# Optimization experiments

Measured on AMD Instinct MI355X. Metric: run time of the kernel, lower is better.

## Reference

```python
import jax, jax.numpy as jnp
import numpy as np

T, D, H, KEXP = 91, 256, 4, 4
DH = D // H
NA, NRG = 128, 1024
NEG = -1e10
SCALE = 2.0  # sqrt(head_num=4), faithful to the original (NOT sqrt(dh))


def _ln(x, g, b, eps=1e-5):
    m = jnp.mean(x, axis=-1, keepdims=True)
    v = jnp.mean((x - m) ** 2, axis=-1, keepdims=True)
    return (x - m) * jax.lax.rsqrt(v + eps) * g + b


def setup_inputs() -> dict:
    key = jax.random.key(0)
    ks = jax.random.split(key, 16)
    s = lambda fan_in: 1.0 / np.sqrt(fan_in)
    inp = {
        "agent": jax.random.normal(ks[0], (NA, T, D), jnp.float32),
        "rg": jax.random.normal(ks[1], (NRG, T, D), jnp.float32),
        "ln_x_g": jnp.ones((D,), jnp.float32),
        "ln_x_b": jnp.zeros((D,), jnp.float32),
        "wk": jax.random.uniform(ks[2], (D, D), jnp.float32, -s(D), s(D)),
        "bk": jnp.zeros((D,), jnp.float32),
        "wv": jax.random.uniform(ks[3], (D, D), jnp.float32, -s(D), s(D)),
        "bv": jnp.zeros((D,), jnp.float32),
        "wq": jax.random.uniform(ks[4], (D, D), jnp.float32, -s(D), s(D)),
        "bq": jnp.zeros((D,), jnp.float32),
        "q_scale": jnp.full((DH,), 0.001, jnp.float32),
        "wy": jax.random.uniform(ks[5], (D, D), jnp.float32, -s(D), s(D)),
        "by": jnp.zeros((D,), jnp.float32),
        "wf1": jax.random.uniform(ks[6], (D, KEXP * D), jnp.float32, -s(D), s(D)),
        "bf1": jnp.zeros((KEXP * D,), jnp.float32),
        "wf2": jax.random.uniform(ks[7], (KEXP * D, D), jnp.float32, -s(KEXP * D), s(KEXP * D)),
        "bf2": jnp.zeros((D,), jnp.float32),
        "ln_z_g": jnp.ones((D,), jnp.float32),
        "ln_z_b": jnp.zeros((D,), jnp.float32),
        "agent_rg_mask": jax.random.randint(ks[8], (T, NA, NRG), 0, 2).astype(bool),
        "padding_mask": jax.random.randint(ks[9], (T, NRG), 0, 2).astype(bool),
        "rg_valid_mask": jax.random.randint(ks[10], (T, NA), 0, 2).astype(bool),
    }
    return inp


def reference(agent, rg, ln_x_g, ln_x_b, wk, bk, wv, bv, wq, bq, q_scale,
              wy, by, wf1, bf1, wf2, bf2, ln_z_g, ln_z_b,
              agent_rg_mask, padding_mask, rg_valid_mask):
    agent_n = _ln(agent, ln_x_g, ln_x_b)   # (Na, T, D)
    rg_n = _ln(rg, ln_x_g, ln_x_b)         # (Nrg, T, D)

    K = jax.nn.relu(rg_n @ wk + bk).reshape(NRG, T, H, DH)
    V = jax.nn.relu(rg_n @ wv + bv).reshape(NRG, T, H, DH)
    Q = jax.nn.relu(agent_n @ wq + bq).reshape(NA, T, H, DH) * q_scale

    # energy: (T, H, Na, Nrg)
    energy = jnp.einsum("athd,rthd->thar", Q, K) / SCALE
    energy = jnp.where(agent_rg_mask[:, None, :, :], energy, NEG)
    energy = jnp.where(padding_mask[:, None, None, :], energy, NEG)
    energy = jnp.where(rg_valid_mask[:, None, :, None], energy, NEG)
    attn = jax.nn.softmax(energy, axis=-1)

    Y1 = jnp.einsum("thar,rthd->athd", attn, V).reshape(NA, T, D)
    Y2 = jax.nn.relu(Y1 @ wy + by)
    S = Y2 + agent_n
    F1 = jax.nn.relu(S @ wf1 + bf1)
    F2 = jax.nn.relu(F1 @ wf2 + bf2)
    Z = _ln(F2, ln_z_g, ln_z_b)

    Qp = jnp.transpose(Q, (1, 2, 0, 3))  # (T,H,Na,dh)
    Kp = jnp.transpose(K, (1, 2, 0, 3))
    Vp = jnp.transpose(V, (1, 2, 0, 3))
    return (Z, Qp, Kp, Vp)
```

## Files before the change

kernel.cpp:

```cpp
#include <hip/hip_runtime.h>

#define T_   91
#define D_   256
#define H_   4
#define DH_  64
#define NA_  128
#define NRG_ 1024
#define KEXP_ 4

typedef float f32x4 __attribute__((ext_vector_type(4)));
typedef short bf16x8 __attribute__((ext_vector_type(8)));

static constexpr float P_EPS = 1.3877787807814457e-17f;

__device__ inline ushort f2bf(float f) {
    union { float f; unsigned u; } v; v.f = f;
    unsigned r = (v.u + 0x7fffu + ((v.u >> 16) & 1u)) >> 16;
    return (ushort)r;
}
__device__ inline unsigned pk2(float a, float b) {
    return (unsigned)f2bf(a) | ((unsigned)f2bf(b) << 16);
}
__device__ inline float bf2f(ushort b) {
    union { unsigned u; float f; } v; v.u = ((unsigned)b) << 16;
    return v.f;
}

#define LN_BLOCKS 2912
#define PM_BLOCKS 2912
#define PW_BLOCKS 3072
#define KV_BLOCKS 2912

__global__ __launch_bounds__(256) void prep_all(
    const float* __restrict__ agent,
    const float* __restrict__ g, const float* __restrict__ b,
    const int* __restrict__ am, const int* __restrict__ pm,
    const int* __restrict__ vmk,
    const float* __restrict__ wk, const float* __restrict__ wv,
    const float* __restrict__ wq, const float* __restrict__ wy,
    const float* __restrict__ wf1, const float* __restrict__ wf2,
    ushort* __restrict__ agn, unsigned* __restrict__ cm,
    ushort* __restrict__ wkvt, ushort* __restrict__ wqt,
    ushort* __restrict__ wyt, ushort* __restrict__ wf1t,
    ushort* __restrict__ wf2t) {
    __shared__ int pmS[NRG_];
    int bid = blockIdx.x;
    if (bid < LN_BLOCKS) {
        int row = bid * 4 + (threadIdx.x >> 6);
        int lane = threadIdx.x & 63;
        f32x4 x = *(const f32x4*)(agent + (size_t)row * D_ + lane * 4);
        float s1 = x[0] + x[1] + x[2] + x[3];
        float s2 = x[0] * x[0] + x[1] * x[1] + x[2] * x[2] + x[3] * x[3];
#pragma unroll
        for (int off = 1; off < 64; off <<= 1) {
            s1 += __shfl_xor(s1, off);
            s2 += __shfl_xor(s2, off);
        }
        float mean = s1 * (1.0f / 256.0f);
        float var = s2 * (1.0f / 256.0f) - mean * mean;
        float rstd = rsqrtf(var + 1e-5f);
        f32x4 gv = *(const f32x4*)(g + lane * 4);
        f32x4 bv = *(const f32x4*)(b + lane * 4);
        float y0 = (x[0] - mean) * rstd * gv[0] + bv[0];
        float y1 = (x[1] - mean) * rstd * gv[1] + bv[1];
        float y2 = (x[2] - mean) * rstd * gv[2] + bv[2];
        float y3 = (x[3] - mean) * rstd * gv[3] + bv[3];
        *(uint2*)(agn + (size_t)row * D_ + lane * 4) =
            make_uint2(pk2(y0, y1), pk2(y2, y3));
    } else if (bid < LN_BLOCKS + PM_BLOCKS) {
        int base = (bid - LN_BLOCKS) * 4;
        int t = base / NA_;
        int w = threadIdx.x >> 6, lane = threadIdx.x & 63;
#pragma unroll
        for (int i = 0; i < 4; ++i)
            pmS[threadIdx.x + i * 256] = pm[(size_t)t * NRG_ + threadIdx.x + i * 256];
        __syncthreads();
        int idx = base + w;
        int a = idx & (NA_ - 1);
        int valid = vmk[t * NA_ + a];
        const int* amrow = am + (size_t)idx * NRG_;
#pragma unroll
        for (int c = 0; c < 16; ++c) {
            int r = c * 64 + lane;
            bool bit = valid && amrow[r] && pmS[r];
            unsigned long long msk = __ballot(bit);
            if (lane == 0) {
                cm[(size_t)idx * 32 + c * 2]     = (unsigned)msk;
                cm[(size_t)idx * 32 + c * 2 + 1] = (unsigned)(msk >> 32);
            }
        }
    } else {
        int idx = (bid - LN_BLOCKS - PM_BLOCKS) * 256 + threadIdx.x;
        if (idx < 131072) {
            const float* W = (idx < 65536) ? wk : wv;
            int li = idx & 65535;
            int n = li >> 8, k = li & 255;
            wkvt[idx] = f2bf(W[(size_t)k * 256 + n]);
        } else if (idx < 196608) {
            int li = idx - 131072;
            int n = li >> 8, k = li & 255;
            wqt[li] = f2bf(wq[(size_t)k * 256 + n]);
        } else if (idx < 262144) {
            int li = idx - 196608;
            int n = li >> 8, k = li & 255;
            wyt[li] = f2bf(wy[(size_t)k * 256 + n]);
        } else if (idx < 524288) {
            int li = idx - 262144;
            int n = li >> 8, k = li & 255;
            wf1t[li] = f2bf(wf1[(size_t)k * 1024 + n]);
        } else {
            int li = idx - 524288;
            int n = li >> 10, k = li & 1023;
            wf2t[li] = f2bf(wf2[(size_t)k * 256 + n]);
        }
    }
}

__global__ __launch_bounds__(512) void gemm_kvq(
    const float* __restrict__ rgf, const ushort* __restrict__ agn,
    const float* __restrict__ lng, const float* __restrict__ lnb,
    const ushort* __restrict__ wkvt, const ushort* __restrict__ wqt,
    const float* __restrict__ bk, const float* __restrict__ bv,
    const float* __restrict__ bq, const float* __restrict__ qs,
    float* __restrict__ Kp, float* __restrict__ Vp, float* __restrict__ Qp,
    ushort* __restrict__ Kb, ushort* __restrict__ Vtb, ushort* __restrict__ Qb) {
    __shared__ ushort Asf[64][264];
    __shared__ ushort Bs[256][72];

    int bid = blockIdx.x;
    bool isQ = bid >= KV_BLOCKS;
    int bxi = 0, t, rb = 0, a0 = 0;
    if (!isQ) {
        int sub = bid & 15, pid = bid >> 4;
        bxi = sub >> 3;
        int by = pid * 8 + (sub & 7);
        t = by >> 4; rb = (by & 15) << 6;
    } else {
        int qid = bid - KV_BLOCKS;
        t = qid >> 1; a0 = (qid & 1) << 6;
    }
    const ushort* Bt = isQ ? wqt : (wkvt + (size_t)(bxi << 8) * 256);

    int tid = threadIdx.x;
    int w = tid >> 6, lane = tid & 63;
    int wm = w >> 2, wn = w & 3;
    int l15 = lane & 15, l4 = lane >> 4;

    if (!isQ) {
        int row = tid >> 3, l8 = tid & 7;
        const float* ap = rgf + ((size_t)(rb + row) * T_ + t) * 256;
        f32x4 xr[8];
#pragma unroll
        for (int c = 0; c < 8; ++c) xr[c] = *(const f32x4*)(ap + l8 * 4 + c * 32);
        float s1 = 0.0f, s2 = 0.0f;
#pragma unroll
        for (int c = 0; c < 8; ++c)
#pragma unroll
            for (int r = 0; r < 4; ++r) { s1 += xr[c][r]; s2 += xr[c][r] * xr[c][r]; }
#pragma unroll
        for (int off = 1; off < 8; off <<= 1) {
            s1 += __shfl_xor(s1, off);
            s2 += __shfl_xor(s2, off);
        }
        float mean = s1 * (1.0f / 256.0f);
        float var = s2 * (1.0f / 256.0f) - mean * mean;
        float rstd = rsqrtf(var + 1e-5f);
#pragma unroll
        for (int c = 0; c < 8; ++c) {
            int col = l8 * 4 + c * 32;
            f32x4 g4 = *(const f32x4*)(lng + col);
            f32x4 b4 = *(const f32x4*)(lnb + col);
            float y0 = (xr[c][0] - mean) * rstd * g4[0] + b4[0];
            float y1 = (xr[c][1] - mean) * rstd * g4[1] + b4[1];
            float y2 = (xr[c][2] - mean) * rstd * g4[2] + b4[2];
            float y3 = (xr[c][3] - mean) * rstd * g4[3] + b4[3];
            *(uint2*)&Asf[row][col] = make_uint2(pk2(y0, y1), pk2(y2, y3));
        }
    } else {
#pragma unroll
        for (int i2 = 0; i2 < 4; ++i2) {
            int chunk = tid + i2 * 512;
            int row = chunk >> 5, c8 = (chunk & 31) * 8;
            *(bf16x8*)&Asf[row][c8] =
                *(const bf16x8*)(agn + ((size_t)(a0 + row) * T_ + t) * 256 + c8);
        }
    }

    f32x4 acc[2][4];
#pragma unroll
    for (int i = 0; i < 2; ++i)
#pragma unroll
        for (int j = 0; j < 4; ++j)
#pragma unroll
            for (int r = 0; r < 4; ++r) acc[i][j][r] = 0.0f;

    for (int k0 = 0; k0 < 256; k0 += 64) {
#pragma unroll
        for (int it = 0; it < 4; ++it) {
            int li = tid + it * 512;
            int row = li >> 3, c8 = (li & 7) * 8;
            *(bf16x8*)&Bs[row][c8] =
                *(const bf16x8*)(Bt + (size_t)row * 256 + k0 + c8);
        }
        __syncthreads();
#pragma unroll
        for (int kk = 0; kk < 2; ++kk) {
            bf16x8 af[2], bfr[4];
#pragma unroll
            for (int i = 0; i < 2; ++i)
                af[i] = *(const bf16x8*)&Asf[wm * 32 + i * 16 + l15][k0 + kk * 32 + l4 * 8];
#pragma unroll
            for (int j = 0; j < 4; ++j)
                bfr[j] = *(const bf16x8*)&Bs[wn * 64 + j * 16 + l15][kk * 32 + l4 * 8];
#pragma unroll
            for (int i = 0; i < 2; ++i)
#pragma unroll
                for (int j = 0; j < 4; ++j)
                    acc[i][j] = __builtin_amdgcn_mfma_f32_16x16x32_bf16(
                        af[i], bfr[j], acc[i][j], 0, 0, 0);
        }
        __syncthreads();
    }

#pragma unroll
    for (int i = 0; i < 2; ++i)
#pragma unroll
        for (int j = 0; j < 4; ++j) {
            int n = wn * 64 + j * 16 + l15;
            int h = n >> 6, d = n & 63;
            int m0 = wm * 32 + i * 16 + l4 * 4;
            float vv[4];
#pragma unroll
            for (int reg = 0; reg < 4; ++reg) {
                float bs = isQ ? bq[n] : (bxi ? bv[n] : bk[n]);
                float x = fmaxf(acc[i][j][reg] + bs, 0.0f);
                if (isQ) x *= qs[d];
                vv[reg] = x;
            }
            if (isQ) {
                size_t base = (((size_t)t * H_ + h) * NA_ + a0) * DH_ + d;
#pragma unroll
                for (int reg = 0; reg < 4; ++reg) {
                    Qp[base + (size_t)(m0 + reg) * DH_] = vv[reg];
                    Qb[base + (size_t)(m0 + reg) * DH_] = f2bf(vv[reg] * 0.5f);
                }
            } else if (!bxi) {
                size_t base = (((size_t)t * H_ + h) * NRG_ + rb) * DH_ + d;
#pragma unroll
                for (int reg = 0; reg < 4; ++reg) {
                    Kp[base + (size_t)(m0 + reg) * DH_] = vv[reg];
                    Kb[base + (size_t)(m0 + reg) * DH_] = f2bf(vv[reg]);
                }
            } else {
                size_t base = (((size_t)t * H_ + h) * NRG_ + rb) * DH_ + d;
#pragma unroll
                for (int reg = 0; reg < 4; ++reg)
                    Vp[base + (size_t)(m0 + reg) * DH_] = vv[reg];
                size_t tb = ((size_t)t * H_ + h) * DH_ * NRG_;
                *(uint2*)(Vtb + tb + (size_t)d * NRG_ + rb + m0) =
                    make_uint2(pk2(vv[0], vv[1]), pk2(vv[2], vv[3]));
            }
        }
}

__global__ __launch_bounds__(512) void gemm_wide(
    const ushort* __restrict__ Ab, const ushort* __restrict__ Bt,
    const float* __restrict__ bias0, const float* __restrict__ bias1,
    const float* __restrict__ aux0, const ushort* __restrict__ residb,
    float* __restrict__ out0, ushort* __restrict__ out2,
    int N, int K, int mode) {
    __shared__ ushort smem[64 * 72 + 256 * 72];
    __shared__ float lnp[2][64][4];
    ushort (*As)[72] = (ushort(*)[72])smem;
    ushort (*Bs)[72] = (ushort(*)[72])(smem + 64 * 72);
    float (*Et)[68] = (float(*)[68])smem;

    int bxi = blockIdx.x, by = blockIdx.y;
    int bn = bxi * 256, bm = by * 64;

    int tid = threadIdx.x;
    int w = tid >> 6, lane = tid & 63;
    int wm = w >> 2, wn = w & 3;
    int l15 = lane & 15, l4 = lane >> 4;

    f32x4 acc[2][4];
#pragma unroll
    for (int i = 0; i < 2; ++i)
#pragma unroll
        for (int j = 0; j < 4; ++j)
#pragma unroll
            for (int r = 0; r < 4; ++r) acc[i][j][r] = 0.0f;

    for (int k0 = 0; k0 < K; k0 += 64) {
        {
            int row = tid >> 3, c8 = (tid & 7) * 8;
            *(bf16x8*)&As[row][c8] =
                *(const bf16x8*)(Ab + (size_t)(bm + row) * K + k0 + c8);
        }
#pragma unroll
        for (int it = 0; it < 4; ++it) {
            int li = tid + it * 512;
            int row = li >> 3, c8 = (li & 7) * 8;
            *(bf16x8*)&Bs[row][c8] =
                *(const bf16x8*)(Bt + (size_t)(bn + row) * K + k0 + c8);
        }
        __syncthreads();
#pragma unroll
        for (int kk = 0; kk < 2; ++kk) {
            bf16x8 af[2], bfr[4];
#pragma unroll
            for (int i = 0; i < 2; ++i)
                af[i] = *(const bf16x8*)&As[wm * 32 + i * 16 + l15][kk * 32 + l4 * 8];
#pragma unroll
            for (int j = 0; j < 4; ++j)
                bfr[j] = *(const bf16x8*)&Bs[wn * 64 + j * 16 + l15][kk * 32 + l4 * 8];
#pragma unroll
            for (int i = 0; i < 2; ++i)
#pragma unroll
                for (int j = 0; j < 4; ++j)
                    acc[i][j] = __builtin_amdgcn_mfma_f32_16x16x32_bf16(
                        af[i], bfr[j], acc[i][j], 0, 0, 0);
        }
        __syncthreads();
    }

    float v[2][4][4];
#pragma unroll
    for (int i = 0; i < 2; ++i)
#pragma unroll
        for (int j = 0; j < 4; ++j)
#pragma unroll
            for (int reg = 0; reg < 4; ++reg) {
                int nl = wn * 64 + j * 16 + l15;
                int rowl = wm * 32 + i * 16 + l4 * 4 + reg;
                float bs = (mode == 0) ? bias0[bn + nl] : bias0[nl];
                float x = fmaxf(acc[i][j][reg] + bs, 0.0f);
                if (mode == 3) x += bf2f(residb[(size_t)(bm + rowl) * 256 + nl]);
                v[i][j][reg] = x;
            }

    if (mode == 5) {
        float rs_[2][4], rq_[2][4];
#pragma unroll
        for (int i = 0; i < 2; ++i)
#pragma unroll
            for (int reg = 0; reg < 4; ++reg) {
                float s = 0.0f, q = 0.0f;
#pragma unroll
                for (int j = 0; j < 4; ++j) {
                    float x = v[i][j][reg];
                    s += x; q += x * x;
                }
#pragma unroll
                for (int off = 1; off < 16; off <<= 1) {
                    s += __shfl_xor(s, off);
                    q += __shfl_xor(q, off);
                }
                rs_[i][reg] = s; rq_[i][reg] = q;
            }
        if (l15 == 0) {
#pragma unroll
            for (int i = 0; i < 2; ++i)
#pragma unroll
                for (int reg = 0; reg < 4; ++reg) {
                    int row = wm * 32 + i * 16 + l4 * 4 + reg;
                    lnp[0][row][wn] = rs_[i][reg];
                    lnp[1][row][wn] = rq_[i][reg];
                }
        }
        __syncthreads();
#pragma unroll
        for (int i = 0; i < 2; ++i)
#pragma unroll
            for (int reg = 0; reg < 4; ++reg) {
                int row = wm * 32 + i * 16 + l4 * 4 + reg;
                float S1 = lnp[0][row][0] + lnp[0][row][1] + lnp[0][row][2] + lnp[0][row][3];
                float S2 = lnp[1][row][0] + lnp[1][row][1] + lnp[1][row][2] + lnp[1][row][3];
                float mean = S1 * (1.0f / 256.0f);
                float var = S2 * (1.0f / 256.0f) - mean * mean;
                float rstd = rsqrtf(var + 1e-5f);
#pragma unroll
                for (int j = 0; j < 4; ++j) {
                    int nl = wn * 64 + j * 16 + l15;
                    float z = (v[i][j][reg] - mean) * rstd * bias1[nl] + aux0[nl];
                    out0[(size_t)(bm + row) * 256 + nl] = z;
                }
            }
        return;
    }

#pragma unroll 1
    for (int jq = 0; jq < 4; ++jq) {
        __syncthreads();
        if (wn == jq) {
#pragma unroll
            for (int i = 0; i < 2; ++i)
#pragma unroll
                for (int j = 0; j < 4; ++j)
#pragma unroll
                    for (int reg = 0; reg < 4; ++reg)
                        Et[wm * 32 + i * 16 + l4 * 4 + reg][j * 16 + l15] = v[i][j][reg];
        }
        __syncthreads();
#pragma unroll
        for (int it = 0; it < 2; ++it) {
            int slot = it * 512 + tid;
            int row = slot >> 4, c4 = (slot & 15) * 4;
            uint2 u = make_uint2(pk2(Et[row][c4], Et[row][c4 + 1]),
                                 pk2(Et[row][c4 + 2], Et[row][c4 + 3]));
            *(uint2*)(out2 + (size_t)(bm + row) * N + bn + jq * 64 + c4) = u;
        }
    }
}

__global__ __launch_bounds__(512) void attn_flash(
    const ushort* __restrict__ Qb, const ushort* __restrict__ Kb,
    const ushort* __restrict__ Vtb, const unsigned* __restrict__ cm,
    ushort* __restrict__ Y1b) {
    int th = blockIdx.x;
    int t = th >> 2, h = th & 3;
    int tid = threadIdx.x;
    int w = tid >> 6, lane = tid & 63;
    int l15 = lane & 15, l4 = lane >> 4;

    __shared__ ushort Ks[2][64][72];
    __shared__ ushort Vts[2][64][72];
    __shared__ ushort Ps[128][72];
    __shared__ unsigned cmAll[128][33];

    bf16x8 qf[2];
#pragma unroll
    for (int kk = 0; kk < 2; ++kk)
        qf[kk] = *(const bf16x8*)(Qb + ((size_t)th * NA_ + w * 16 + l15) * DH_
                                  + kk * 32 + l4 * 8);

    {
        const uint4* src = (const uint4*)(cm + (size_t)t * NA_ * 32 + tid * 8);
        uint4 c0 = src[0], c1 = src[1];
        int a = tid >> 2, wd = (tid & 3) * 8;
        cmAll[a][wd + 0] = c0.x; cmAll[a][wd + 1] = c0.y;
        cmAll[a][wd + 2] = c0.z; cmAll[a][wd + 3] = c0.w;
        cmAll[a][wd + 4] = c1.x; cmAll[a][wd + 5] = c1.y;
        cmAll[a][wd + 6] = c1.z; cmAll[a][wd + 7] = c1.w;
    }

    int srow = tid >> 3, sc8 = (tid & 7) * 8;
    const ushort* Kbase = Kb + (size_t)th * NRG_ * DH_;
    const ushort* Vbase = Vtb + (size_t)th * DH_ * NRG_;
    bf16x8 kreg = *(const bf16x8*)(Kbase + (size_t)srow * DH_ + sc8);
    bf16x8 vreg = *(const bf16x8*)(Vbase + (size_t)srow * NRG_ + sc8);
    *(bf16x8*)&Ks[0][srow][sc8] = kreg;
    *(bf16x8*)&Vts[0][srow][sc8] = vreg;
    __syncthreads();

    f32x4 o[4];
    float rsum[4] = {0.0f, 0.0f, 0.0f, 0.0f};
#pragma unroll
    for (int ds = 0; ds < 4; ++ds)
#pragma unroll
        for (int r = 0; r < 4; ++r) o[ds][r] = 0.0f;

    for (int rt = 0; rt < 16; ++rt) {
        int cur = rt & 1;
        if (rt < 15) {
            int r0n = (rt + 1) * 64;
            kreg = *(const bf16x8*)(Kbase + (size_t)(r0n + srow) * DH_ + sc8);
            vreg = *(const bf16x8*)(Vbase + (size_t)srow * NRG_ + r0n + sc8);
        }

        f32x4 e[4];
#pragma unroll
        for (int rs = 0; rs < 4; ++rs) {
#pragma unroll
            for (int r = 0; r < 4; ++r) e[rs][r] = 0.0f;
#pragma unroll
            for (int kk = 0; kk < 2; ++kk) {
                bf16x8 kf = *(const bf16x8*)&Ks[cur][rs * 16 + l15][kk * 32 + l4 * 8];
                e[rs] = __builtin_amdgcn_mfma_f32_16x16x32_bf16(qf[kk], kf, e[rs], 0, 0, 0);
            }
        }

#pragma unroll
        for (int reg = 0; reg < 4; ++reg) {
            int a_loc = w * 16 + l4 * 4 + reg;
            unsigned w0 = cmAll[a_loc][rt * 2], w1 = cmAll[a_loc][rt * 2 + 1];
#pragma unroll
            for (int rs = 0; rs < 4; ++rs) {
                unsigned wd = (rs & 2) ? w1 : w0;
                int bit = (wd >> ((rs & 1) * 16 + l15)) & 1;
                float p = bit ? __expf(e[rs][reg]) : P_EPS;
                rsum[reg] += p;
                Ps[a_loc][rs * 16 + l15] = f2bf(p);
            }
        }

#pragma unroll
        for (int rc = 0; rc < 2; ++rc) {
            bf16x8 pa = *(const bf16x8*)&Ps[w * 16 + l15][rc * 32 + l4 * 8];
#pragma unroll
            for (int ds = 0; ds < 4; ++ds) {
                bf16x8 vf = *(const bf16x8*)&Vts[cur][ds * 16 + l15][rc * 32 + l4 * 8];
                o[ds] = __builtin_amdgcn_mfma_f32_16x16x32_bf16(pa, vf, o[ds], 0, 0, 0);
            }
        }

        if (rt < 15) {
            *(bf16x8*)&Ks[cur ^ 1][srow][sc8] = kreg;
            *(bf16x8*)&Vts[cur ^ 1][srow][sc8] = vreg;
            __syncthreads();
        }
    }

#pragma unroll
    for (int off = 1; off < 16; off <<= 1)
#pragma unroll
        for (int reg = 0; reg < 4; ++reg)
            rsum[reg] += __shfl_xor(rsum[reg], off);
    float rinv[4];
#pragma unroll
    for (int reg = 0; reg < 4; ++reg) rinv[reg] = 1.0f / rsum[reg];

#pragma unroll
    for (int ds = 0; ds < 4; ++ds)
#pragma unroll
        for (int reg = 0; reg < 4; ++reg) {
            int a_g = w * 16 + l4 * 4 + reg;
            int d = ds * 16 + l15;
            Y1b[((size_t)a_g * T_ + t) * D_ + h * DH_ + d] = f2bf(o[ds][reg] * rinv[reg]);
        }
}

extern "C" void kernel_launch(void* const* d_in, const int* in_sizes, int n_in,
                              void* d_out, int out_size, void* d_ws, size_t ws_size,
                              hipStream_t stream) {
    const float* agent   = (const float*)d_in[0];
    const float* rg      = (const float*)d_in[1];
    const float* ln_x_g  = (const float*)d_in[2];
    const float* ln_x_b  = (const float*)d_in[3];
    const float* wk      = (const float*)d_in[4];
    const float* bk      = (const float*)d_in[5];
    const float* wv      = (const float*)d_in[6];
    const float* bv      = (const float*)d_in[7];
    const float* wq      = (const float*)d_in[8];
    const float* bq      = (const float*)d_in[9];
    const float* q_scale = (const float*)d_in[10];
    const float* wy      = (const float*)d_in[11];
    const float* by      = (const float*)d_in[12];
    const float* wf1     = (const float*)d_in[13];
    const float* bf1     = (const float*)d_in[14];
    const float* wf2     = (const float*)d_in[15];
    const float* bf2     = (const float*)d_in[16];
    const float* ln_z_g  = (const float*)d_in[17];
    const float* ln_z_b  = (const float*)d_in[18];
    const int*   am      = (const int*)d_in[19];
    const int*   pm      = (const int*)d_in[20];
    const int*   vmk     = (const int*)d_in[21];

    float* Z  = (float*)d_out;
    float* Qp = Z + (size_t)NA_ * T_ * D_;
    float* Kp = Qp + (size_t)NA_ * T_ * D_;
    float* Vp = Kp + (size_t)NRG_ * T_ * D_;

    char* p = (char*)d_ws;
    ushort* agn_b = (ushort*)p;   p += (size_t)NA_ * T_ * D_ * 2;
    ushort* wkvt  = (ushort*)p;   p += (size_t)512 * 256 * 2;
    ushort* wqt   = (ushort*)p;   p += (size_t)256 * 256 * 2;
    ushort* wyt   = (ushort*)p;   p += (size_t)256 * 256 * 2;
    ushort* wf1t  = (ushort*)p;   p += (size_t)1024 * 256 * 2;
    ushort* wf2t  = (ushort*)p;   p += (size_t)256 * 1024 * 2;
    unsigned* cm  = (unsigned*)p; p += (size_t)T_ * NA_ * 32 * 4;
    ushort* Kb    = (ushort*)p;   p += (size_t)T_ * H_ * NRG_ * DH_ * 2;
    ushort* Vtb   = (ushort*)p;   p += (size_t)T_ * H_ * NRG_ * DH_ * 2;
    ushort* Qb    = (ushort*)p;   p += (size_t)T_ * H_ * NA_ * DH_ * 2;
    ushort* Y1b   = (ushort*)p;   p += (size_t)NA_ * T_ * D_ * 2;
    ushort* Sb    = (ushort*)p;   p += (size_t)NA_ * T_ * D_ * 2;
    ushort* F1b   = (ushort*)p;   p += (size_t)NA_ * T_ * D_ * KEXP_ * 2;

    prep_all<<<dim3(LN_BLOCKS + PM_BLOCKS + PW_BLOCKS), dim3(256), 0, stream>>>(
        agent, ln_x_g, ln_x_b, am, pm, vmk,
        wk, wv, wq, wy, wf1, wf2,
        agn_b, cm, wkvt, wqt, wyt, wf1t, wf2t);

    gemm_kvq<<<dim3(KV_BLOCKS + T_ * 2), dim3(512), 0, stream>>>(
        rg, agn_b, ln_x_g, ln_x_b, wkvt, wqt, bk, bv, bq, q_scale,
        Kp, Vp, Qp, Kb, Vtb, Qb);

    attn_flash<<<dim3(T_ * H_), dim3(512), 0, stream>>>(Qb, Kb, Vtb, cm, Y1b);

    gemm_wide<<<dim3(1, NA_ * T_ / 64), dim3(512), 0, stream>>>(
        Y1b, wyt, by, nullptr, nullptr, agn_b,
        nullptr, Sb, 256, 256, 3);

    gemm_wide<<<dim3(4, NA_ * T_ / 64), dim3(512), 0, stream>>>(
        Sb, wf1t, bf1, nullptr, nullptr, nullptr,
        nullptr, F1b, 1024, 256, 0);

    gemm_wide<<<dim3(1, NA_ * T_ / 64), dim3(512), 0, stream>>>(
        F1b, wf2t, bf2, ln_z_g, ln_z_b, nullptr,
        Z, nullptr, 256, 1024, 5);
}
```

Measured before the change: 242.0 us.

## Make K/V projection GEMM persistent with register prefetch of next rg tile

The K/V part of gemm_kvq now runs as 512 persistent blocks, each looping over several of the 2912 tiles in strided order, while Q tiles keep one block each. Each iteration loads the next tile's raw fp32 rg rows into registers before the current tile's MFMA loop, so the global load overlaps with compute and the LayerNorm stats. This cuts block launch overhead and hides load latency. In exchange the B-weight tiles are still reloaded per tile, xr registers stay live across the GEMM, and load balance is coarser since each block handles 5 or 6 tiles.

```diff
diff --git a/kernel.cpp b/kernel.cpp
--- a/kernel.cpp
+++ b/kernel.cpp
@@ -29,7 +29,8 @@
 #define LN_BLOCKS 2912
 #define PM_BLOCKS 2912
 #define PW_BLOCKS 3072
-#define KV_BLOCKS 2912
+#define KV_TILES  2912
+#define PERS      512
 
 __global__ __launch_bounds__(256) void prep_all(
     const float* __restrict__ agent,
@@ -128,30 +129,91 @@
     __shared__ ushort Bs[256][72];
 
     int bid = blockIdx.x;
-    bool isQ = bid >= KV_BLOCKS;
-    int bxi = 0, t, rb = 0, a0 = 0;
-    if (!isQ) {
-        int sub = bid & 15, pid = bid >> 4;
-        bxi = sub >> 3;
-        int by = pid * 8 + (sub & 7);
-        t = by >> 4; rb = (by & 15) << 6;
-    } else {
-        int qid = bid - KV_BLOCKS;
-        t = qid >> 1; a0 = (qid & 1) << 6;
-    }
-    const ushort* Bt = isQ ? wqt : (wkvt + (size_t)(bxi << 8) * 256);
-
     int tid = threadIdx.x;
     int w = tid >> 6, lane = tid & 63;
     int wm = w >> 2, wn = w & 3;
     int l15 = lane & 15, l4 = lane >> 4;
 
-    if (!isQ) {
-        int row = tid >> 3, l8 = tid & 7;
-        const float* ap = rgf + ((size_t)(rb + row) * T_ + t) * 256;
-        f32x4 xr[8];
+    if (bid >= PERS) {
+        int qid = bid - PERS;
+        int t = qid >> 1, a0 = (qid & 1) << 6;
+#pragma unroll
+        for (int i2 = 0; i2 < 4; ++i2) {
+            int chunk = tid + i2 * 512;
+            int row = chunk >> 5, c8 = (chunk & 31) * 8;
+            *(bf16x8*)&Asf[row][c8] =
+                *(const bf16x8*)(agn + ((size_t)(a0 + row) * T_ + t) * 256 + c8);
+        }
+        f32x4 acc[2][4];
+#pragma unroll
+        for (int i = 0; i < 2; ++i)
+#pragma unroll
+            for (int j = 0; j < 4; ++j)
+#pragma unroll
+                for (int r = 0; r < 4; ++r) acc[i][j][r] = 0.0f;
+        for (int k0 = 0; k0 < 256; k0 += 64) {
+#pragma unroll
+            for (int it = 0; it < 4; ++it) {
+                int li = tid + it * 512;
+                int row = li >> 3, c8 = (li & 7) * 8;
+                *(bf16x8*)&Bs[row][c8] =
+                    *(const bf16x8*)(wqt + (size_t)row * 256 + k0 + c8);
+            }
+            __syncthreads();
+#pragma unroll
+            for (int kk = 0; kk < 2; ++kk) {
+                bf16x8 af[2], bfr[4];
+#pragma unroll
+                for (int i = 0; i < 2; ++i)
+                    af[i] = *(const bf16x8*)&Asf[wm * 32 + i * 16 + l15][k0 + kk * 32 + l4 * 8];
+#pragma unroll
+                for (int j = 0; j < 4; ++j)
+                    bfr[j] = *(const bf16x8*)&Bs[wn * 64 + j * 16 + l15][kk * 32 + l4 * 8];
+#pragma unroll
+                for (int i = 0; i < 2; ++i)
+#pragma unroll
+                    for (int j = 0; j < 4; ++j)
+                        acc[i][j] = __builtin_amdgcn_mfma_f32_16x16x32_bf16(
+                            af[i], bfr[j], acc[i][j], 0, 0, 0);
+            }
+            __syncthreads();
+        }
+#pragma unroll
+        for (int i = 0; i < 2; ++i)
+#pragma unroll
+            for (int j = 0; j < 4; ++j) {
+                int n = wn * 64 + j * 16 + l15;
+                int h = n >> 6, d = n & 63;
+                int m0 = wm * 32 + i * 16 + l4 * 4;
+                size_t base = (((size_t)t * H_ + h) * NA_ + a0) * DH_ + d;
+#pragma unroll
+                for (int reg = 0; reg < 4; ++reg) {
+                    float x = fmaxf(acc[i][j][reg] + bq[n], 0.0f) * qs[d];
+                    Qp[base + (size_t)(m0 + reg) * DH_] = x;
+                    Qb[base + (size_t)(m0 + reg) * DH_] = f2bf(x * 0.5f);
+                }
+            }
+        return;
+    }
+
+    int p = bid;
+    int nt = (KV_TILES - p + PERS - 1) / PERS;
+    int arow = tid >> 3, l8 = tid & 7;
+
+    int cb = p;
+    int sub = cb & 15, pid = cb >> 4;
+    int bxi = sub >> 3;
+    int by = pid * 8 + (sub & 7);
+    int t = by >> 4, rb = (by & 15) << 6;
+
+    f32x4 xr[8];
+    {
+        const float* ap = rgf + ((size_t)(rb + arow) * T_ + t) * 256;
 #pragma unroll
         for (int c = 0; c < 8; ++c) xr[c] = *(const f32x4*)(ap + l8 * 4 + c * 32);
+    }
+
+    for (int it = 0; it < nt; ++it) {
         float s1 = 0.0f, s2 = 0.0f;
 #pragma unroll
         for (int c = 0; c < 8; ++c)
@@ -174,93 +236,90 @@
             float y1 = (xr[c][1] - mean) * rstd * g4[1] + b4[1];
             float y2 = (xr[c][2] - mean) * rstd * g4[2] + b4[2];
             float y3 = (xr[c][3] - mean) * rstd * g4[3] + b4[3];
-            *(uint2*)&Asf[row][col] = make_uint2(pk2(y0, y1), pk2(y2, y3));
-        }
-    } else {
-#pragma unroll
-        for (int i2 = 0; i2 < 4; ++i2) {
-            int chunk = tid + i2 * 512;
-            int row = chunk >> 5, c8 = (chunk & 31) * 8;
-            *(bf16x8*)&Asf[row][c8] =
-                *(const bf16x8*)(agn + ((size_t)(a0 + row) * T_ + t) * 256 + c8);
-        }
-    }
-
-    f32x4 acc[2][4];
-#pragma unroll
-    for (int i = 0; i < 2; ++i)
-#pragma unroll
-        for (int j = 0; j < 4; ++j)
-#pragma unroll
-            for (int r = 0; r < 4; ++r) acc[i][j][r] = 0.0f;
-
-    for (int k0 = 0; k0 < 256; k0 += 64) {
-#pragma unroll
-        for (int it = 0; it < 4; ++it) {
-            int li = tid + it * 512;
-            int row = li >> 3, c8 = (li & 7) * 8;
-            *(bf16x8*)&Bs[row][c8] =
-                *(const bf16x8*)(Bt + (size_t)row * 256 + k0 + c8);
+            *(uint2*)&Asf[arow][col] = make_uint2(pk2(y0, y1), pk2(y2, y3));
+        }
+
+        int nbxi = 0, nt_ = 0, nrb = 0;
+        if (it + 1 < nt) {
+            int nb = p + (it + 1) * PERS;
+            int nsub = nb & 15, npid = nb >> 4;
+            nbxi = nsub >> 3;
+            int nby = npid * 8 + (nsub & 7);
+            nt_ = nby >> 4; nrb = (nby & 15) << 6;
+            const float* apn = rgf + ((size_t)(nrb + arow) * T_ + nt_) * 256;
+#pragma unroll
+            for (int c = 0; c < 8; ++c) xr[c] = *(const f32x4*)(apn + l8 * 4 + c * 32);
         }
         __syncthreads();
-#pragma unroll
-        for (int kk = 0; kk < 2; ++kk) {
-            bf16x8 af[2], bfr[4];
-#pragma unroll
-            for (int i = 0; i < 2; ++i)
-                af[i] = *(const bf16x8*)&Asf[wm * 32 + i * 16 + l15][k0 + kk * 32 + l4 * 8];
+
+        const ushort* Bt = wkvt + (size_t)(bxi << 8) * 256;
+        f32x4 acc[2][4];
+#pragma unroll
+        for (int i = 0; i < 2; ++i)
 #pragma unroll
             for (int j = 0; j < 4; ++j)
-                bfr[j] = *(const bf16x8*)&Bs[wn * 64 + j * 16 + l15][kk * 32 + l4 * 8];
-#pragma unroll
-            for (int i = 0; i < 2; ++i)
+#pragma unroll
+                for (int r = 0; r < 4; ++r) acc[i][j][r] = 0.0f;
+
+        for (int k0 = 0; k0 < 256; k0 += 64) {
+#pragma unroll
+            for (int it2 = 0; it2 < 4; ++it2) {
+                int li = tid + it2 * 512;
+                int row = li >> 3, c8 = (li & 7) * 8;
+                *(bf16x8*)&Bs[row][c8] =
+                    *(const bf16x8*)(Bt + (size_t)row * 256 + k0 + c8);
+            }
+            __syncthreads();
+#pragma unroll
+            for (int kk = 0; kk < 2; ++kk) {
+                bf16x8 af[2], bfr[4];
+#pragma unroll
+                for (int i = 0; i < 2; ++i)
+                    af[i] = *(const bf16x8*)&Asf[wm * 32 + i * 16 + l15][k0 + kk * 32 + l4 * 8];
 #pragma unroll
                 for (int j = 0; j < 4; ++j)
-                    acc[i][j] = __builtin_amdgcn_mfma_f32_16x16x32_bf16(
-                        af[i], bfr[j], acc[i][j], 0, 0, 0);
-        }
-        __syncthreads();
-    }
-
-#pragma unroll
-    for (int i = 0; i < 2; ++i)
-#pragma unroll
-        for (int j = 0; j < 4; ++j) {
-            int n = wn * 64 + j * 16 + l15;
-            int h = n >> 6, d = n & 63;
-            int m0 = wm * 32 + i * 16 + l4 * 4;
-            float vv[4];
-#pragma unroll
-            for (int reg = 0; reg < 4; ++reg) {
-                float bs = isQ ? bq[n] : (bxi ? bv[n] : bk[n]);
-                float x = fmaxf(acc[i][j][reg] + bs, 0.0f);
-                if (isQ) x *= qs[d];
-                vv[reg] = x;
-            }
-            if (isQ) {
-                size_t base = (((size_t)t * H_ + h) * NA_ + a0) * DH_ + d;
-#pragma unroll
-                for (int reg = 0; reg < 4; ++reg) {
-                    Qp[base + (size_t)(m0 + reg) * DH_] = vv[reg];
-                    Qb[base + (size_t)(m0 + reg) * DH_] = f2bf(vv[reg] * 0.5f);
+                    bfr[j] = *(const bf16x8*)&Bs[wn * 64 + j * 16 + l15][kk * 32 + l4 * 8];
+#pragma unroll
+                for (int i = 0; i < 2; ++i)
+#pragma unroll
+                    for (int j = 0; j < 4; ++j)
+                        acc[i][j] = __builtin_amdgcn_mfma_f32_16x16x32_bf16(
+                            af[i], bfr[j], acc[i][j], 0, 0, 0);
+            }
+            __syncthreads();
+        }
+
+#pragma unroll
+        for (int i = 0; i < 2; ++i)
+#pragma unroll
+            for (int j = 0; j < 4; ++j) {
+                int n = wn * 64 + j * 16 + l15;
+                int h = n >> 6, d = n & 63;
+                int m0 = wm * 32 + i * 16 + l4 * 4;
+                float vv[4];
+#pragma unroll
+                for (int reg = 0; reg < 4; ++reg)
+                    vv[reg] = fmaxf(acc[i][j][reg] + (bxi ? bv[n] : bk[n]), 0.0f);
+                if (!bxi) {
+                    size_t base = (((size_t)t * H_ + h) * NRG_ + rb) * DH_ + d;
+#pragma unroll
+                    for (int reg = 0; reg < 4; ++reg) {
+                        Kp[base + (size_t)(m0 + reg) * DH_] = vv[reg];
+                        Kb[base + (size_t)(m0 + reg) * DH_] = f2bf(vv[reg]);
+                    }
+                } else {
+                    size_t base = (((size_t)t * H_ + h) * NRG_ + rb) * DH_ + d;
+#pragma unroll
+                    for (int reg = 0; reg < 4; ++reg)
+                        Vp[base + (size_t)(m0 + reg) * DH_] = vv[reg];
+                    size_t tb = ((size_t)t * H_ + h) * DH_ * NRG_;
+                    *(uint2*)(Vtb + tb + (size_t)d * NRG_ + rb + m0) =
+                        make_uint2(pk2(vv[0], vv[1]), pk2(vv[2], vv[3]));
                 }
-            } else if (!bxi) {
-                size_t base = (((size_t)t * H_ + h) * NRG_ + rb) * DH_ + d;
-#pragma unroll
-                for (int reg = 0; reg < 4; ++reg) {
-                    Kp[base + (size_t)(m0 + reg) * DH_] = vv[reg];
-                    Kb[base + (size_t)(m0 + reg) * DH_] = f2bf(vv[reg]);
-                }
-            } else {
-                size_t base = (((size_t)t * H_ + h) * NRG_ + rb) * DH_ + d;
-#pragma unroll
-                for (int reg = 0; reg < 4; ++reg)
-                    Vp[base + (size_t)(m0 + reg) * DH_] = vv[reg];
-                size_t tb = ((size_t)t * H_ + h) * DH_ * NRG_;
-                *(uint2*)(Vtb + tb + (size_t)d * NRG_ + rb + m0) =
-                    make_uint2(pk2(vv[0], vv[1]), pk2(vv[2], vv[3]));
-            }
-        }
+            }
+
+        bxi = nbxi; t = nt_; rb = nrb;
+    }
 }
 
 __global__ __launch_bounds__(512) void gemm_wide(
@@ -581,7 +640,7 @@
         wk, wv, wq, wy, wf1, wf2,
         agn_b, cm, wkvt, wqt, wyt, wf1t, wf2t);
 
-    gemm_kvq<<<dim3(KV_BLOCKS + T_ * 2), dim3(512), 0, stream>>>(
+    gemm_kvq<<<dim3(PERS + T_ * 2), dim3(512), 0, stream>>>(
         rg, agn_b, ln_x_g, ln_x_b, wkvt, wqt, bk, bv, bq, q_scale,
         Kp, Vp, Qp, Kb, Vtb, Qb);
 
```

New measurement: 260.1 us. +7.5%, slower.
